# Optimization experiments

Measured on AMD Instinct MI355X. Metric: run time of the kernel, lower is better.

The kernel has to match this reference:

```python
import jax, jax.numpy as jnp
import numpy as np

B, T, NCH, DFF = 64, 480, 32, 32   # batch, seq_len+pred_len, d_model, d_ff
LAYERS = 3                          # conv_layers
NFFT, WIN, HOP = 64, 64, 4
FRAMES = T // HOP + 1               # 121 == (seq_len+pred_len+hop)/hop


def _stft(x):
    # x: [B, N, T] real -> (re, im) each [B, N, NFFT, FRAMES]
    # torch.stft(center=True, pad_mode='reflect', normalized=True, onesided=False)
    pad = NFFT // 2
    xp = jnp.pad(x, ((0, 0), (0, 0), (pad, pad)), mode='reflect')
    idx = jnp.arange(FRAMES)[:, None] * HOP + jnp.arange(NFFT)[None, :]
    win = 0.5 * (1.0 - jnp.cos(2.0 * jnp.pi * jnp.arange(WIN, dtype=jnp.float32) / WIN))  # periodic hann
    frames = xp[:, :, idx] * win                      # [B, N, FRAMES, NFFT]
    spec = jnp.fft.fft(frames, axis=-1) / jnp.sqrt(jnp.float32(NFFT))
    spec = jnp.swapaxes(spec, -1, -2)                 # [B, N, NFFT, FRAMES]
    return spec.real.astype(x.dtype), spec.imag.astype(x.dtype)


def _conv2d(x, w, b, dil, pad):
    y = jax.lax.conv_general_dilated(
        x, w, window_strides=(1, 1), padding=[(pad, pad), (pad, pad)],
        rhs_dilation=(dil, dil), dimension_numbers=('NCHW', 'OIHW', 'NCHW'))
    return y + b[None, :, None, None]


def _cconv(xr, xi, wr, wi, br, bi, dil, pad):
    # apply_complexConv2D: fr(re) - fi(im) + 1j*(fr(im) + fi(re)), biases included in each apply
    rr = _conv2d(xr, wr, br, dil, pad)
    ri = _conv2d(xi, wr, br, dil, pad)
    ir = _conv2d(xr, wi, bi, dil, pad)
    ii = _conv2d(xi, wi, bi, dil, pad)
    return rr - ii, ri + ir


def _cmul(order, ar, ai, br, bi):
    return (jnp.einsum(order, ar, br) - jnp.einsum(order, ai, bi),
            jnp.einsum(order, ar, bi) + jnp.einsum(order, ai, br))


def reference(x, w0r, w0i, b0r, b0i, W1r, W1i, B1r, B1i, W2r, W2i, B2r, B2i, w_l0, b_l0, w_l2, b_l2):
    xt = jnp.swapaxes(x, 1, 2)                         # [B, N, T]
    sr, si = _stft(xt)                                 # [B, N, F, K]
    qkr, qki = _cmul('bnfk,bngk->bnfg', sr, si, sr, si)
    qkr, qki = jax.nn.sigmoid(qkr), jax.nn.sigmoid(qki)
    ar, ai = _cmul('bnfg,bngk->bnfk', qkr, qki, sr, si)

    outs_r, outs_i = [], []
    r0, i0 = _cconv(ar, ai, w0r, w0i, b0r, b0i, 1, 0)  # 1x1 complex conv
    outs_r.append(jax.nn.relu(r0)); outs_i.append(jax.nn.relu(i0))
    for k in range(1, LAYERS):                          # dilated 3x3 complex conv pairs
        j = k - 1
        hr, hi = _cconv(ar, ai, W1r[j], W1i[j], B1r[j], B1i[j], k, k)
        hr, hi = _cconv(hr, hi, W2r[j], W2i[j], B2r[j], B2i[j], k, k)
        outs_r.append(jax.nn.relu(hr)); outs_i.append(jax.nn.relu(hi))
    mr = sum(outs_r) / LAYERS
    mi = sum(outs_i) / LAYERS

    # l0: Linear(2 -> 1) over stacked [real, imag]
    cr = mr * w_l0[0, 0] + mi * w_l0[0, 1] + b_l0[0]    # [B, N, F, K]
    h = cr.mean(axis=2)                                 # [B, N, K]
    y = jnp.einsum('bnk,tk->bnt', h, w_l2) + b_l2       # l2: Linear(FRAMES -> T)
    return jnp.transpose(y, (0, 2, 1))                  # [B, T, N]


def setup_inputs() -> dict:
    key = jax.random.key(0)
    ks = jax.random.split(key, 18)
    s1 = 1.0 / np.sqrt(NCH)          # 1x1 conv fan-in
    s3 = 1.0 / np.sqrt(NCH * 9)      # 3x3 conv fan-in
    return {
        'x':   jax.random.normal(ks[0], (B, T, NCH), jnp.float32),
        'w0r': jax.random.normal(ks[1], (NCH, NCH, 1, 1), jnp.float32) * s1,
        'w0i': jax.random.normal(ks[2], (NCH, NCH, 1, 1), jnp.float32) * s1,
        'b0r': jax.random.normal(ks[3], (NCH,), jnp.float32) * 0.01,
        'b0i': jax.random.normal(ks[4], (NCH,), jnp.float32) * 0.01,
        'W1r': jax.random.normal(ks[5], (LAYERS - 1, DFF, NCH, 3, 3), jnp.float32) * s3,
        'W1i': jax.random.normal(ks[6], (LAYERS - 1, DFF, NCH, 3, 3), jnp.float32) * s3,
        'B1r': jax.random.normal(ks[7], (LAYERS - 1, DFF), jnp.float32) * 0.01,
        'B1i': jax.random.normal(ks[8], (LAYERS - 1, DFF), jnp.float32) * 0.01,
        'W2r': jax.random.normal(ks[9], (LAYERS - 1, NCH, DFF, 3, 3), jnp.float32) * s3,
        'W2i': jax.random.normal(ks[10], (LAYERS - 1, NCH, DFF, 3, 3), jnp.float32) * s3,
        'B2r': jax.random.normal(ks[11], (LAYERS - 1, NCH), jnp.float32) * 0.01,
        'B2i': jax.random.normal(ks[12], (LAYERS - 1, NCH), jnp.float32) * 0.01,
        'w_l0': jax.random.normal(ks[13], (1, 2), jnp.float32) * 0.5,
        'b_l0': jax.random.normal(ks[14], (1,), jnp.float32) * 0.01,
        'w_l2': jax.random.normal(ks[15], (T, FRAMES), jnp.float32) * (1.0 / np.sqrt(FRAMES)),
        'b_l2': jax.random.normal(ks[16], (T,), jnp.float32) * 0.01,
    }
```

## Files before the change

kernel.cpp:

```cpp
#include <hip/hip_runtime.h>
#include <hip/hip_bf16.h>


typedef __attribute__((ext_vector_type(8))) short bf16x8;
typedef __attribute__((ext_vector_type(4))) short bf16x4;
typedef __attribute__((ext_vector_type(4))) float f32x4;

__device__ __forceinline__ ushort f2bf(float v) {
  __hip_bfloat16 h = __float2bfloat16(v);
  return *reinterpret_cast<ushort*>(&h);
}
__device__ __forceinline__ float bf2f_raw(ushort u) {
  union { uint i; float f; } c; c.i = ((uint)u) << 16; return c.f;
}
__device__ __forceinline__ void split_bf(float v, ushort& h, ushort& l) {
  h = f2bf(v); l = f2bf(v - bf2f_raw(h));
}
__device__ __forceinline__ bf16x8 mk8(bf16x4 a, bf16x4 b) {
  bf16x8 r;
  r[0]=a[0]; r[1]=a[1]; r[2]=a[2]; r[3]=a[3];
  r[4]=b[0]; r[5]=b[1]; r[6]=b[2]; r[7]=b[3];
  return r;
}
__device__ __forceinline__ void gld16(const ushort* g, char* lds) {
  __builtin_amdgcn_global_load_lds(
      (const __attribute__((address_space(1))) void*)g,
      (__attribute__((address_space(3))) void*)lds, 16, 0, 0);
}

#define MFMA16(A,B,C) __builtin_amdgcn_mfma_f32_16x16x32_bf16(A, B, C, 0, 0, 0)
#define SPMACC(acc, Ah, Al, Bh, Bl)      \
  acc = MFMA16(Ah, Bh, acc);             \
  acc = MFMA16(Al, Bh, acc);             \
  acc = MFMA16(Ah, Bl, acc);

__global__ __launch_bounds__(512) void stft_mfma_k(const float* __restrict__ x,
                                                   const ushort* __restrict__ WF,
                                                   ushort* __restrict__ ap) {
  __shared__ __align__(16) char smem[133376];
  const int bid = blockIdx.x;
  const int b = bid >> 5, n = bid & 31;
  const int tid = threadIdx.x;
  ushort* xph = reinterpret_cast<ushort*>(smem + 131072);
  ushort* xpl = xph + 576;

  for (int i = tid; i < 576; i += 512) {
    float v = 0.f;
    if (i < 544) {
      int p = i - 32;
      if (p < 0) p = -p;
      if (p >= 480) p = 958 - p;
      v = x[(b * 480 + p) * 32 + n];
    }
    ushort h, l; split_bf(v, h, l);
    xph[i] = h; xpl[i] = l;
  }
  __syncthreads();

  const int wv = tid >> 6, lane = tid & 63;
  const int mt = wv >> 1, nth = wv & 1;
  const int l15 = lane & 15, l4 = lane >> 4;

  bf16x8 WA[2][2][2];
#pragma unroll
  for (int cs = 0; cs < 2; ++cs)
#pragma unroll
    for (int part = 0; part < 2; ++part)
#pragma unroll
      for (int ks = 0; ks < 2; ++ks)
        WA[cs][part][ks] = *reinterpret_cast<const bf16x8*>(
            WF + (((cs * 2 + part) * 2 + ks) * 4 + mt) * 512 + lane * 8);

  f32x4 acc1[2][4];
#pragma unroll
  for (int cs = 0; cs < 2; ++cs)
#pragma unroll
    for (int nt = 0; nt < 4; ++nt) acc1[cs][nt] = (f32x4){0.f, 0.f, 0.f, 0.f};

#pragma unroll
  for (int ks = 0; ks < 2; ++ks) {
    bf16x8 bh[4], bl[4];
#pragma unroll
    for (int nt = 0; nt < 4; ++nt) {
      int n_ = ((nth * 4 + nt) * 16) + l15;
      int e = n_ * 4 + ks * 32 + l4 * 8;
      bf16x4 h0 = *reinterpret_cast<const bf16x4*>(xph + e);
      bf16x4 h1 = *reinterpret_cast<const bf16x4*>(xph + e + 4);
      bf16x4 l0 = *reinterpret_cast<const bf16x4*>(xpl + e);
      bf16x4 l1 = *reinterpret_cast<const bf16x4*>(xpl + e + 4);
      bh[nt] = mk8(h0, h1); bl[nt] = mk8(l0, l1);
    }
#pragma unroll
    for (int cs = 0; cs < 2; ++cs)
#pragma unroll
      for (int nt = 0; nt < 4; ++nt) {
        SPMACC(acc1[cs][nt], WA[cs][0][ks], WA[cs][1][ks], bh[nt], bl[nt]);
      }
  }

#pragma unroll
  for (int cs = 0; cs < 2; ++cs)
#pragma unroll
    for (int nt = 0; nt < 4; ++nt) {
      int k = (nth * 4 + nt) * 16 + l15;
      bool kv = (k < 121);
#pragma unroll
      for (int r = 0; r < 4; ++r) {
        int f = mt * 16 + l4 * 4 + r;
        float v = kv ? acc1[cs][nt][r] : 0.f;
        ushort h, l; split_bf(v, h, l);
        int ba = (f << 8) + (k << 1); ba ^= (f & 7) << 4;
        *reinterpret_cast<ushort*>(smem + cs * 32768 + ba) = h;
        *reinterpret_cast<ushort*>(smem + cs * 32768 + 16384 + ba) = l;
        int bt = (k << 7) + (f << 1); bt ^= (k & 7) << 4;
        *reinterpret_cast<ushort*>(smem + 65536 + cs * 32768 + bt) = h;
        *reinterpret_cast<ushort*>(smem + 65536 + cs * 32768 + 16384 + bt) = l;
      }
    }
  __syncthreads();

  f32x4 acc2[2][4];
#pragma unroll
  for (int nt = 0; nt < 2; ++nt)
#pragma unroll
    for (int c = 0; c < 4; ++c) acc2[nt][c] = (f32x4){0.f, 0.f, 0.f, 0.f};

#pragma unroll
  for (int ks = 0; ks < 4; ++ks) {
    bf16x8 A_[2][2];
#pragma unroll
    for (int comp = 0; comp < 2; ++comp)
#pragma unroll
      for (int part = 0; part < 2; ++part) {
        int f = mt * 16 + l15;
        int ba = (f << 8) + ((ks * 32 + l4 * 8) << 1); ba ^= (f & 7) << 4;
        A_[comp][part] = *reinterpret_cast<const bf16x8*>(smem + comp * 32768 + part * 16384 + ba);
      }
    bf16x8 B_[2][2][2];
#pragma unroll
    for (int comp = 0; comp < 2; ++comp)
#pragma unroll
      for (int part = 0; part < 2; ++part)
#pragma unroll
        for (int nt = 0; nt < 2; ++nt) {
          int g = (nth * 2 + nt) * 16 + l15;
          int ba = (g << 8) + ((ks * 32 + l4 * 8) << 1); ba ^= (g & 7) << 4;
          B_[comp][part][nt] = *reinterpret_cast<const bf16x8*>(smem + comp * 32768 + part * 16384 + ba);
        }
#pragma unroll
    for (int nt = 0; nt < 2; ++nt) {
      SPMACC(acc2[nt][0], A_[0][0], A_[0][1], B_[0][0][nt], B_[0][1][nt]);
      SPMACC(acc2[nt][1], A_[1][0], A_[1][1], B_[1][0][nt], B_[1][1][nt]);
      SPMACC(acc2[nt][2], A_[0][0], A_[0][1], B_[1][0][nt], B_[1][1][nt]);
      SPMACC(acc2[nt][3], A_[1][0], A_[1][1], B_[0][0][nt], B_[0][1][nt]);
    }
  }
  __syncthreads();

#pragma unroll
  for (int nt = 0; nt < 2; ++nt) {
    int g = (nth * 2 + nt) * 16 + l15;
#pragma unroll
    for (int r = 0; r < 4; ++r) {
      int f = mt * 16 + l4 * 4 + r;
      float qr = acc2[nt][0][r] - acc2[nt][1][r];
      float qi = acc2[nt][2][r] + acc2[nt][3][r];
      float vr = 1.f / (1.f + __expf(-qr));
      float vi = 1.f / (1.f + __expf(-qi));
      int ba = (f << 7) + (g << 1); ba ^= (f & 7) << 4;
      ushort h, l;
      split_bf(vr, h, l);
      *reinterpret_cast<ushort*>(smem + ba) = h;
      *reinterpret_cast<ushort*>(smem + 8192 + ba) = l;
      split_bf(vi, h, l);
      *reinterpret_cast<ushort*>(smem + 16384 + ba) = h;
      *reinterpret_cast<ushort*>(smem + 24576 + ba) = l;
    }
  }
  __syncthreads();

  f32x4 acc3[4][3];
#pragma unroll
  for (int nt = 0; nt < 4; ++nt)
#pragma unroll
    for (int c = 0; c < 3; ++c) acc3[nt][c] = (f32x4){0.f, 0.f, 0.f, 0.f};

#pragma unroll
  for (int ks = 0; ks < 2; ++ks) {
    bf16x8 QA[2][2];
#pragma unroll
    for (int comp = 0; comp < 2; ++comp)
#pragma unroll
      for (int part = 0; part < 2; ++part) {
        int f = mt * 16 + l15;
        int ba = (f << 7) + ((ks * 32 + l4 * 8) << 1); ba ^= (f & 7) << 4;
        QA[comp][part] = *reinterpret_cast<const bf16x8*>(smem + comp * 16384 + part * 8192 + ba);
      }
#pragma unroll
    for (int nt = 0; nt < 4; ++nt) {
      int k = (nth * 4 + nt) * 16 + l15;
      int bq = (k << 7) + ((ks * 32 + l4 * 8) << 1); bq ^= (k & 7) << 4;
      bf16x8 Srh = *reinterpret_cast<const bf16x8*>(smem + 65536 + bq);
      bf16x8 Srl = *reinterpret_cast<const bf16x8*>(smem + 81920 + bq);
      bf16x8 Sih = *reinterpret_cast<const bf16x8*>(smem + 98304 + bq);
      bf16x8 Sil = *reinterpret_cast<const bf16x8*>(smem + 114688 + bq);
      SPMACC(acc3[nt][0], QA[0][0], QA[0][1], Srh, Srl);
      SPMACC(acc3[nt][1], QA[1][0], QA[1][1], Sih, Sil);
      SPMACC(acc3[nt][2], QA[0][0], QA[0][1], Sih, Sil);
      SPMACC(acc3[nt][2], QA[1][0], QA[1][1], Srh, Srl);
    }
  }
  __syncthreads();

#pragma unroll
  for (int nt = 0; nt < 4; ++nt) {
    int k = (nth * 4 + nt) * 16 + l15;
#pragma unroll
    for (int r = 0; r < 4; ++r) {
      int f = mt * 16 + l4 * 4 + r;
      float ar = acc3[nt][0][r] - acc3[nt][1][r];
      float ai = acc3[nt][2][r];
      int ba = (f << 8) + (k << 1); ba ^= (f & 7) << 4;
      *reinterpret_cast<ushort*>(smem + ba) = f2bf(ar);
      *reinterpret_cast<ushort*>(smem + 16384 + ba) = f2bf(ai);
    }
  }
  __syncthreads();

  uint4* dst = reinterpret_cast<uint4*>(ap);
  for (int i = tid; i < 2048; i += 512) {
    int comp = i >> 10, rem = i & 1023;
    int f = rem >> 4, q = rem & 15;
    uint4 v = *reinterpret_cast<const uint4*>(
        smem + comp * 16384 + (f << 8) + ((q ^ (f & 7)) << 4));
    dst[((size_t)(b * 64 + n + 32 * comp) * 64) * 16 + rem] = v;
  }
}

__global__ __launch_bounds__(256) void transpose_k(const ushort* __restrict__ ap,
    ushort* __restrict__ an, const ushort* __restrict__ AF,
    const float* __restrict__ BB, const float* __restrict__ wl0,
    float* __restrict__ csumA) {
  __shared__ __align__(16) ushort T[64 * 128];
  const int b = blockIdx.x >> 6, h = blockIdx.x & 63;
  const int tid = threadIdx.x;
#pragma unroll
  for (int it = 0; it < 4; ++it) {
    int i = it * 256 + tid;
    int cc = i >> 4, q = i & 15;
    const uint4* src = reinterpret_cast<const uint4*>(ap) +
                       ((size_t)((b * 64 + cc) * 64 + h) * 16 + q);
    *reinterpret_cast<uint4*>(&T[cc * 128 + q * 8]) = *src;
  }
  __syncthreads();
  const int p = tid >> 1, cc0 = (tid & 1) * 32;
  uint ou[16];
#pragma unroll
  for (int it = 0; it < 16; ++it) {
    uint lo = T[(cc0 + 2 * it) * 128 + p];
    uint hi = T[(cc0 + 2 * it + 1) * 128 + p];
    ou[it] = lo | (hi << 16);
  }
  uint4* dst = reinterpret_cast<uint4*>(an + ((size_t)((b * 64 + h) * 128 + p) * 64 + cc0));
#pragma unroll
  for (int r = 0; r < 4; ++r) dst[r] = make_uint4(ou[4*r], ou[4*r+1], ou[4*r+2], ou[4*r+3]);
  __syncthreads();

  char* S = reinterpret_cast<char*>(T);
#pragma unroll
  for (int it = 0; it < 16; ++it) {
    int byt = p * 128 + (cc0 + 2 * it) * 2;
    byt ^= (p & 7) << 4;
    *reinterpret_cast<uint*>(S + byt) = ou[it];
  }
  __syncthreads();

  const int wave = tid >> 6, lane = tid & 63;
  const int mtb = wave & 1, ntb = (wave >> 1) * 4;
  const int l15 = lane & 15, l4 = lane >> 4;
  const ushort* Ab = AF + lane * 8;
  bf16x8 AH[2][2], AL[2][2];
#pragma unroll
  for (int ks = 0; ks < 2; ++ks)
#pragma unroll
    for (int mi = 0; mi < 2; ++mi) {
      AH[ks][mi] = *reinterpret_cast<const bf16x8*>(Ab + ks * 2048 + (mtb + 2 * mi) * 512);
      AL[ks][mi] = *reinterpret_cast<const bf16x8*>(Ab + 4096 + ks * 2048 + (mtb + 2 * mi) * 512);
    }
  f32x4 acc[2][4];
#pragma unroll
  for (int mi = 0; mi < 2; ++mi)
#pragma unroll
    for (int nt = 0; nt < 4; ++nt) acc[mi][nt] = (f32x4){0.f, 0.f, 0.f, 0.f};
#pragma unroll
  for (int ks = 0; ks < 2; ++ks) {
    bf16x8 bv[4];
#pragma unroll
    for (int nt = 0; nt < 4; ++nt) {
      int w = (ntb + nt) * 16 + l15;
      int byt = w * 128 + ks * 64 + l4 * 16;
      byt ^= (w & 7) << 4;
      bv[nt] = *reinterpret_cast<const bf16x8*>(S + byt);
    }
#pragma unroll
    for (int nt = 0; nt < 4; ++nt) {
      acc[0][nt] = MFMA16(AH[ks][0], bv[nt], acc[0][nt]);
      acc[1][nt] = MFMA16(AH[ks][1], bv[nt], acc[1][nt]);
    }
#pragma unroll
    for (int nt = 0; nt < 4; ++nt) {
      acc[0][nt] = MFMA16(AL[ks][0], bv[nt], acc[0][nt]);
      acc[1][nt] = MFMA16(AL[ks][1], bv[nt], acc[1][nt]);
    }
  }
  const float w00 = wl0[0], w01 = wl0[1];
#pragma unroll
  for (int nt = 0; nt < 4; ++nt) {
    int gw = (ntb + nt) * 16 + l15;
    if (gw < 121) {
#pragma unroll
      for (int r = 0; r < 4; ++r) {
        int n = mtb * 16 + l4 * 4 + r;
        float rr = acc[0][nt][r] + BB[n];
        float im = acc[1][nt][r] + BB[n + 32];
        csumA[((size_t)(b * 32 + n) * 64 + h) * 121 + gw] =
            (fmaxf(rr, 0.f) * w00 + fmaxf(im, 0.f) * w01) * (1.f / 3.f);
      }
    }
  }
}

__global__ __launch_bounds__(256) void prep_k(
    const float* __restrict__ w0r, const float* __restrict__ w0i,
    const float* __restrict__ b0r, const float* __restrict__ b0i,
    const float* __restrict__ W1r, const float* __restrict__ W1i,
    const float* __restrict__ B1r, const float* __restrict__ B1i,
    const float* __restrict__ W2r, const float* __restrict__ W2i,
    const float* __restrict__ B2r, const float* __restrict__ B2i,
    const float* __restrict__ wl2,
    ushort* __restrict__ AF, ushort* __restrict__ WF, float* __restrict__ BB,
    float* __restrict__ wl2T, float* __restrict__ zpg) {
  const int blk = blockIdx.x, tid = threadIdx.x;
  const float PI32 = 0.0981747704246810387f;

  if (blk == 38) {
    for (int i = tid; i < 121 * 480; i += 256) {
      int k = i / 480, t = i - k * 480;
      wl2T[i] = wl2[t * 121 + k];
    }
    if (tid < 16) zpg[tid] = 0.f;
    return;
  }
  if (blk == 37) {
    for (int i = tid; i < 16384; i += 256) {
      int j = i & 7, ln = (i >> 3) & 63, mt = (i >> 9) & 3, ks = (i >> 11) & 1;
      int part = (i >> 12) & 1, cs = (i >> 13) & 1;
      int f = mt * 16 + (ln & 15);
      int t = ks * 32 + (ln >> 4) * 8 + j;
      float win = 0.5f * (1.0f - __cosf(PI32 * (float)t));
      int m = (f * t) & 63;
      float sv, cv;
      __sincosf(PI32 * (float)m, &sv, &cv);
      float val = (cs == 0) ? (win * cv * 0.125f) : (-win * sv * 0.125f);
      ushort h = f2bf(val);
      WF[i] = part ? f2bf(val - bf2f_raw(h)) : h;
    }
    return;
  }

  int conv, tap, TT;
  const float *Wr, *Wi;
  if (blk == 0) { conv = 0; tap = 0; TT = 1; Wr = w0r; Wi = w0i; }
  else {
    int q = blk - 1; conv = 1 + q / 9; tap = q - (q / 9) * 9; TT = 9;
    if (conv == 1)      { Wr = W1r;        Wi = W1i; }
    else if (conv == 2) { Wr = W2r;        Wi = W2i; }
    else if (conv == 3) { Wr = W1r + 9216; Wi = W1i + 9216; }
    else                { Wr = W2r + 9216; Wi = W2i + 9216; }
  }
  ushort thi[16], tlo[16];
#pragma unroll
  for (int jj = 0; jj < 16; ++jj) {
    int e = tid * 16 + jj;
    int j = e & 7, lane_e = (e >> 3) & 63, mt = (e >> 9) & 3, ks = (e >> 11) & 1;
    int o  = mt * 16 + (lane_e & 15);
    int cc = ks * 32 + 8 * (lane_e >> 4) + j;
    int ci = cc & 31, ch = cc >> 5, on = o & 31, oh = o >> 5;
    float wr = Wr[(on * 32 + ci) * TT + tap];
    float wi = Wi[(on * 32 + ci) * TT + tap];
    float v = (oh == 0) ? (ch == 0 ? wr : -wi) : (ch == 0 ? wi : wr);
    ushort h = f2bf(v);
    thi[jj] = h;
    tlo[jj] = f2bf(v - bf2f_raw(h));
  }
  ushort* base = AF + conv * 73728 + tap * 8192 + tid * 16;
  uint4* dh = reinterpret_cast<uint4*>(base);
  uint4* dl = reinterpret_cast<uint4*>(base + 4096);
  dh[0] = *reinterpret_cast<uint4*>(&thi[0]);
  dh[1] = *reinterpret_cast<uint4*>(&thi[8]);
  dl[0] = *reinterpret_cast<uint4*>(&tlo[0]);
  dl[1] = *reinterpret_cast<uint4*>(&tlo[8]);

  if (blk == 0) {
    for (int i = tid; i < 320; i += 256) {
      int c = i >> 6, o = i & 63;
      const float *br, *bi;
      if (c == 0)      { br = b0r;      bi = b0i; }
      else if (c == 1) { br = B1r;      bi = B1i; }
      else if (c == 2) { br = B2r;      bi = B2i; }
      else if (c == 3) { br = B1r + 32; bi = B1i + 32; }
      else             { br = B2r + 32; bi = B2i + 32; }
      BB[c * 64 + o] = (o < 32) ? (br[o] - bi[o]) : (br[o - 32] + bi[o - 32]);
    }
  }
}

#define RWB 8704

__device__ __forceinline__ void run_taps9(const char* __restrict__ smem,
    const ushort* __restrict__ afrag, int d,
    int ng, int mtb, int l15, int l4, int lane, f32x4 acc[2][8]) {
  const ushort* Ab = afrag + lane * 8;
#pragma unroll
  for (int t = 0; t < 9; ++t) {
    const int dy = t / 3;
    const int dxo = ((t - dy * 3) - 1) * d;
    const int bufb = (dy - 1) * d + 2 + ng * 2;
    const ushort* At = Ab + t * 8192;
    bf16x8 AH[2][2], AL[2][2];
#pragma unroll
    for (int ks = 0; ks < 2; ++ks)
#pragma unroll
      for (int mi = 0; mi < 2; ++mi) {
        AH[ks][mi] = *reinterpret_cast<const bf16x8*>(At + ks * 2048 + (mtb + 2 * mi) * 512);
        AL[ks][mi] = *reinterpret_cast<const bf16x8*>(At + 4096 + ks * 2048 + (mtb + 2 * mi) * 512);
      }
#pragma unroll
    for (int ks = 0; ks < 2; ++ks) {
      bf16x8 bv[8];
#pragma unroll
      for (int nt = 0; nt < 8; ++nt) {
        int bw = (nt & 3) * 16 + l15 + dxo + 2;
        int byt = (bufb + (nt >> 2)) * RWB + bw * 128 + ks * 64 + l4 * 16;
        byt ^= (bw & 7) << 4;
        bv[nt] = *reinterpret_cast<const bf16x8*>(smem + byt);
      }
      __builtin_amdgcn_s_setprio(1);
#pragma unroll
      for (int nt = 0; nt < 8; ++nt) {
        acc[0][nt] = MFMA16(AH[ks][0], bv[nt], acc[0][nt]);
        acc[1][nt] = MFMA16(AH[ks][1], bv[nt], acc[1][nt]);
      }
#pragma unroll
      for (int nt = 0; nt < 8; ++nt) {
        acc[0][nt] = MFMA16(AL[ks][0], bv[nt], acc[0][nt]);
        acc[1][nt] = MFMA16(AL[ks][1], bv[nt], acc[1][nt]);
      }
      __builtin_amdgcn_s_setprio(0);
    }
  }
}

__device__ __forceinline__ void conv_body3(char* smem,
    const ushort* __restrict__ xin, ushort* __restrict__ tout,
    const ushort* __restrict__ afrag, const float* __restrict__ bb,
    const float* __restrict__ wl0, float* __restrict__ csum,
    const ushort* __restrict__ zp,
    int d, int b, int h0, int side, int mode, int tid) {
  const int wave = tid >> 6, lane = tid & 63;
  const int mtb = wave & 1;
  const int ng = wave >> 1;
  const int l15 = lane & 15, l4 = lane >> 4;
  const int wbase = side * 64;

#pragma unroll
  for (int r = 0; r < 8; ++r) {
    const int hh = h0 + r - 2;
    const bool hv = ((unsigned)hh < 64u);
    const ushort* rowp = xin + ((size_t)(b * 64 + hh) << 13);
#pragma unroll
    for (int c = 0; c < 3; ++c) {
      int i = c * 256 + tid;
      if (i < 544) {
        int bw = i >> 3, q = i & 7;
        int gw = wbase + bw - 2;
        int qs = q ^ (bw & 7);
        const ushort* src = (hv && (unsigned)gw < 128u)
                                ? (rowp + (size_t)gw * 64 + qs * 8)
                                : zp;
        char* ldsb = smem + r * RWB + ((i & ~63) << 4);
        gld16(src, ldsb);
      }
    }
  }
  __syncthreads();

  f32x4 acc[2][8];
#pragma unroll
  for (int mi = 0; mi < 2; ++mi)
#pragma unroll
    for (int nt = 0; nt < 8; ++nt) acc[mi][nt] = (f32x4){0.f, 0.f, 0.f, 0.f};

  run_taps9(smem, afrag, d, ng, mtb, l15, l4, lane, acc);

  if (mode == 2) {
    __syncthreads();
    uint* Lb = reinterpret_cast<uint*>(smem);
#pragma unroll
    for (int mi = 0; mi < 2; ++mi) {
#pragma unroll
      for (int rp = 0; rp < 2; ++rp) {
        int o = (mtb + 2 * mi) * 16 + l4 * 4 + rp * 2;
        float b0 = bb[o], b1 = bb[o + 1];
#pragma unroll
        for (int nt = 0; nt < 8; ++nt) {
          int jrow = ng * 2 + (nt >> 2);
          int wl = (nt & 3) * 16 + l15;
          uint pk = (uint)f2bf(acc[mi][nt][rp * 2] + b0) |
                    ((uint)f2bf(acc[mi][nt][rp * 2 + 1] + b1) << 16);
          Lb[(jrow * 32 + (o >> 1)) * 66 + wl] = pk;
        }
      }
    }
    __syncthreads();
#pragma unroll
    for (int c = 0; c < 8; ++c) {
      int i = c * 256 + tid;
      int jrow = i >> 9, rem = i & 511;
      int wl = rem >> 3, q = rem & 7;
      int gw = wbase + wl;
      int hh = h0 + jrow;
      bool val = (gw < 121);
      uint4 v;
      v.x = val ? Lb[(jrow * 32 + q * 4 + 0) * 66 + wl] : 0u;
      v.y = val ? Lb[(jrow * 32 + q * 4 + 1) * 66 + wl] : 0u;
      v.z = val ? Lb[(jrow * 32 + q * 4 + 2) * 66 + wl] : 0u;
      v.w = val ? Lb[(jrow * 32 + q * 4 + 3) * 66 + wl] : 0u;
      *reinterpret_cast<uint4*>(
          tout + (((size_t)(b * 64 + hh) * 128 + gw) * 64 + q * 8)) = v;
    }
  } else {
    const float w00 = wl0[0], w01 = wl0[1];
#pragma unroll
    for (int nt = 0; nt < 8; ++nt) {
      int gw = wbase + (nt & 3) * 16 + l15;
      int hh = h0 + ng * 2 + (nt >> 2);
      if (gw < 121) {
#pragma unroll
        for (int r = 0; r < 4; ++r) {
          int n = mtb * 16 + l4 * 4 + r;
          float rr = acc[0][nt][r] + bb[n];
          float im = acc[1][nt][r] + bb[n + 32];
          float v = (fmaxf(rr, 0.f) * w00 + fmaxf(im, 0.f) * w01) * (1.f / 3.f);
          float* p = csum + ((size_t)(b * 32 + n) * 64 + hh) * 121 + gw;
          if (mode == 1) v += *p;
          *p = v;
        }
      }
    }
  }
}

__global__ __launch_bounds__(256, 2) void convD1_k(
    const ushort* __restrict__ an, ushort* __restrict__ t1, ushort* __restrict__ t2,
    const ushort* __restrict__ AF, const float* __restrict__ BB,
    const float* __restrict__ wl0, const ushort* __restrict__ zp) {
  __shared__ __align__(16) char smem[8 * RWB];
  const int x = blockIdx.x & 7, j = blockIdx.x >> 3;
  const int role = j & 1, sub = j >> 1;
  const int wg = (x << 8) | sub;
  const int b = wg >> 5, rem = wg & 31;
  const int h0 = ((rem >> 1) & 15) * 4, side = rem & 1;
  const int tid = threadIdx.x;
  if (role == 0)
    conv_body3(smem, an, t1, AF + 1 * 73728, BB + 64, wl0, nullptr, zp, 1, b, h0, side, 2, tid);
  else
    conv_body3(smem, an, t2, AF + 3 * 73728, BB + 192, wl0, nullptr, zp, 2, b, h0, side, 2, tid);
}

__global__ __launch_bounds__(256, 2) void convD2_k(
    const ushort* __restrict__ t1, const ushort* __restrict__ t2,
    const ushort* __restrict__ AF, const float* __restrict__ BB,
    const float* __restrict__ wl0, float* __restrict__ csumA,
    float* __restrict__ csumB, const ushort* __restrict__ zp) {
  __shared__ __align__(16) char smem[8 * RWB];
  const int x = blockIdx.x & 7, j = blockIdx.x >> 3;
  const int role = j & 1, sub = j >> 1;
  const int wg = (x << 8) | sub;
  const int b = wg >> 5, rem = wg & 31;
  const int h0 = ((rem >> 1) & 15) * 4, side = rem & 1;
  const int tid = threadIdx.x;
  if (role == 0)
    conv_body3(smem, t1, nullptr, AF + 2 * 73728, BB + 128, wl0, csumA, zp, 1, b, h0, side, 1, tid);
  else
    conv_body3(smem, t2, nullptr, AF + 4 * 73728, BB + 256, wl0, csumB, zp, 2, b, h0, side, 0, tid);
}

__global__ __launch_bounds__(256) void epi_k(const float* __restrict__ csumA,
    const float* __restrict__ csumB,
    const float* __restrict__ bl0, const float* __restrict__ wl2T,
    const float* __restrict__ bl2, float* __restrict__ out) {
  const int b = blockIdx.x >> 5, n = blockIdx.x & 31;
  __shared__ float sh[121];
  const int tid = threadIdx.x;
  const float* baseA = csumA + (size_t)(b * 32 + n) * 64 * 121;
  const float* baseB = csumB + (size_t)(b * 32 + n) * 64 * 121;
  for (int k = tid; k < 121; k += 256) {
    float s = 0.f;
#pragma unroll 8
    for (int f = 0; f < 64; ++f) s += baseA[f * 121 + k] + baseB[f * 121 + k];
    sh[k] = s * (1.f / 64.f) + bl0[0];
  }
  __syncthreads();
  for (int t = tid; t < 480; t += 256) {
    float acc = bl2[t];
#pragma unroll 8
    for (int k = 0; k < 121; ++k) acc = fmaf(sh[k], wl2T[k * 480 + t], acc);
    out[(b * 480 + t) * 32 + n] = acc;
  }
}

extern "C" void kernel_launch(void* const* d_in, const int* in_sizes, int n_in,
                              void* d_out, int out_size, void* d_ws, size_t ws_size,
                              hipStream_t stream) {
  const float* x   = (const float*)d_in[0];
  const float* w0r = (const float*)d_in[1];
  const float* w0i = (const float*)d_in[2];
  const float* b0r = (const float*)d_in[3];
  const float* b0i = (const float*)d_in[4];
  const float* W1r = (const float*)d_in[5];
  const float* W1i = (const float*)d_in[6];
  const float* B1r = (const float*)d_in[7];
  const float* B1i = (const float*)d_in[8];
  const float* W2r = (const float*)d_in[9];
  const float* W2i = (const float*)d_in[10];
  const float* B2r = (const float*)d_in[11];
  const float* B2i = (const float*)d_in[12];
  const float* wl0 = (const float*)d_in[13];
  const float* bl0 = (const float*)d_in[14];
  const float* wl2 = (const float*)d_in[15];
  const float* bl2 = (const float*)d_in[16];

  char* ws = (char*)d_ws;
  const size_t MB64 = (size_t)64 << 20;
  ushort* ap    = (ushort*)ws;
  ushort* t2    = (ushort*)ws;
  ushort* an    = (ushort*)(ws + MB64);
  float*  csumB = (float*)(ws + MB64);
  ushort* t1    = (ushort*)(ws + 2 * MB64);
  float*  csumA = (float*)(ws + 3 * MB64);
  const size_t CSZ = (size_t)64 * 32 * 64 * 121 * 4;
  ushort* AF   = (ushort*)(ws + 3 * MB64 + CSZ);
  ushort* WFp  = AF + 5 * 73728;
  float*  BB   = (float*)(WFp + 16384);
  float*  wl2T = BB + 320;
  float*  zpg  = wl2T + 58080;
  float*  out  = (float*)d_out;

  hipLaunchKernelGGL(prep_k, dim3(39), dim3(256), 0, stream,
                     w0r, w0i, b0r, b0i, W1r, W1i, B1r, B1i, W2r, W2i, B2r, B2i,
                     wl2, AF, WFp, BB, wl2T, zpg);
  hipLaunchKernelGGL(stft_mfma_k, dim3(2048), dim3(512), 0, stream, x, WFp, ap);
  hipLaunchKernelGGL(transpose_k, dim3(4096), dim3(256), 0, stream,
                     ap, an, AF, BB, wl0, csumA);
  hipLaunchKernelGGL(convD1_k, dim3(4096), dim3(256), 0, stream,
                     an, t1, t2, AF, BB, wl0, (const ushort*)zpg);
  hipLaunchKernelGGL(convD2_k, dim3(4096), dim3(256), 0, stream,
                     t1, t2, AF, BB, wl0, csumA, csumB, (const ushort*)zpg);
  hipLaunchKernelGGL(epi_k, dim3(2048), dim3(256), 0, stream,
                     csumA, csumB, bl0, wl2T, bl2, out);
}
```

Baseline: 501.1 us.

## Share staged input tile across both dilated convs in convD1 and store directly

convD1 now stages each input tile into LDS once and runs both the dilation-1 and dilation-2 convolutions on it inside one block. This halves the grid and removes the duplicate global loads of the shared input. The LDS-transpose epilogue is replaced by direct 8-byte packed bf16 stores from registers to t1/t2, which drops two barriers and the LDS round trip but gives less coalesced global writes. Each block now does twice the MFMA work, so there are fewer blocks available to hide latency.

```diff
diff --git a/kernel.cpp b/kernel.cpp
--- a/kernel.cpp
+++ b/kernel.cpp
@@ -417,62 +417,9 @@
 
 #define RWB 8704
 
-__device__ __forceinline__ void run_taps9(const char* __restrict__ smem,
-    const ushort* __restrict__ afrag, int d,
-    int ng, int mtb, int l15, int l4, int lane, f32x4 acc[2][8]) {
-  const ushort* Ab = afrag + lane * 8;
-#pragma unroll
-  for (int t = 0; t < 9; ++t) {
-    const int dy = t / 3;
-    const int dxo = ((t - dy * 3) - 1) * d;
-    const int bufb = (dy - 1) * d + 2 + ng * 2;
-    const ushort* At = Ab + t * 8192;
-    bf16x8 AH[2][2], AL[2][2];
-#pragma unroll
-    for (int ks = 0; ks < 2; ++ks)
-#pragma unroll
-      for (int mi = 0; mi < 2; ++mi) {
-        AH[ks][mi] = *reinterpret_cast<const bf16x8*>(At + ks * 2048 + (mtb + 2 * mi) * 512);
-        AL[ks][mi] = *reinterpret_cast<const bf16x8*>(At + 4096 + ks * 2048 + (mtb + 2 * mi) * 512);
-      }
-#pragma unroll
-    for (int ks = 0; ks < 2; ++ks) {
-      bf16x8 bv[8];
-#pragma unroll
-      for (int nt = 0; nt < 8; ++nt) {
-        int bw = (nt & 3) * 16 + l15 + dxo + 2;
-        int byt = (bufb + (nt >> 2)) * RWB + bw * 128 + ks * 64 + l4 * 16;
-        byt ^= (bw & 7) << 4;
-        bv[nt] = *reinterpret_cast<const bf16x8*>(smem + byt);
-      }
-      __builtin_amdgcn_s_setprio(1);
-#pragma unroll
-      for (int nt = 0; nt < 8; ++nt) {
-        acc[0][nt] = MFMA16(AH[ks][0], bv[nt], acc[0][nt]);
-        acc[1][nt] = MFMA16(AH[ks][1], bv[nt], acc[1][nt]);
-      }
-#pragma unroll
-      for (int nt = 0; nt < 8; ++nt) {
-        acc[0][nt] = MFMA16(AL[ks][0], bv[nt], acc[0][nt]);
-        acc[1][nt] = MFMA16(AL[ks][1], bv[nt], acc[1][nt]);
-      }
-      __builtin_amdgcn_s_setprio(0);
-    }
-  }
-}
-
-__device__ __forceinline__ void conv_body3(char* smem,
-    const ushort* __restrict__ xin, ushort* __restrict__ tout,
-    const ushort* __restrict__ afrag, const float* __restrict__ bb,
-    const float* __restrict__ wl0, float* __restrict__ csum,
-    const ushort* __restrict__ zp,
-    int d, int b, int h0, int side, int mode, int tid) {
-  const int wave = tid >> 6, lane = tid & 63;
-  const int mtb = wave & 1;
-  const int ng = wave >> 1;
-  const int l15 = lane & 15, l4 = lane >> 4;
-  const int wbase = side * 64;
-
+__device__ __forceinline__ void stage8(char* smem,
+    const ushort* __restrict__ xin, const ushort* __restrict__ zp,
+    int b, int h0, int wbase, int tid) {
 #pragma unroll
   for (int r = 0; r < 8; ++r) {
     const int hh = h0 + r - 2;
@@ -493,70 +440,48 @@
       }
     }
   }
-  __syncthreads();
-
-  f32x4 acc[2][8];
-#pragma unroll
-  for (int mi = 0; mi < 2; ++mi)
-#pragma unroll
-    for (int nt = 0; nt < 8; ++nt) acc[mi][nt] = (f32x4){0.f, 0.f, 0.f, 0.f};
-
-  run_taps9(smem, afrag, d, ng, mtb, l15, l4, lane, acc);
-
-  if (mode == 2) {
-    __syncthreads();
-    uint* Lb = reinterpret_cast<uint*>(smem);
-#pragma unroll
-    for (int mi = 0; mi < 2; ++mi) {
-#pragma unroll
-      for (int rp = 0; rp < 2; ++rp) {
-        int o = (mtb + 2 * mi) * 16 + l4 * 4 + rp * 2;
-        float b0 = bb[o], b1 = bb[o + 1];
-#pragma unroll
-        for (int nt = 0; nt < 8; ++nt) {
-          int jrow = ng * 2 + (nt >> 2);
-          int wl = (nt & 3) * 16 + l15;
-          uint pk = (uint)f2bf(acc[mi][nt][rp * 2] + b0) |
-                    ((uint)f2bf(acc[mi][nt][rp * 2 + 1] + b1) << 16);
-          Lb[(jrow * 32 + (o >> 1)) * 66 + wl] = pk;
-        }
-      }
-    }
-    __syncthreads();
-#pragma unroll
-    for (int c = 0; c < 8; ++c) {
-      int i = c * 256 + tid;
-      int jrow = i >> 9, rem = i & 511;
-      int wl = rem >> 3, q = rem & 7;
-      int gw = wbase + wl;
-      int hh = h0 + jrow;
-      bool val = (gw < 121);
-      uint4 v;
-      v.x = val ? Lb[(jrow * 32 + q * 4 + 0) * 66 + wl] : 0u;
-      v.y = val ? Lb[(jrow * 32 + q * 4 + 1) * 66 + wl] : 0u;
-      v.z = val ? Lb[(jrow * 32 + q * 4 + 2) * 66 + wl] : 0u;
-      v.w = val ? Lb[(jrow * 32 + q * 4 + 3) * 66 + wl] : 0u;
-      *reinterpret_cast<uint4*>(
-          tout + (((size_t)(b * 64 + hh) * 128 + gw) * 64 + q * 8)) = v;
-    }
-  } else {
-    const float w00 = wl0[0], w01 = wl0[1];
-#pragma unroll
-    for (int nt = 0; nt < 8; ++nt) {
-      int gw = wbase + (nt & 3) * 16 + l15;
-      int hh = h0 + ng * 2 + (nt >> 2);
-      if (gw < 121) {
-#pragma unroll
-        for (int r = 0; r < 4; ++r) {
-          int n = mtb * 16 + l4 * 4 + r;
-          float rr = acc[0][nt][r] + bb[n];
-          float im = acc[1][nt][r] + bb[n + 32];
-          float v = (fmaxf(rr, 0.f) * w00 + fmaxf(im, 0.f) * w01) * (1.f / 3.f);
-          float* p = csum + ((size_t)(b * 32 + n) * 64 + hh) * 121 + gw;
-          if (mode == 1) v += *p;
-          *p = v;
-        }
-      }
+}
+
+__device__ __forceinline__ void run_taps9(const char* __restrict__ smem,
+    const ushort* __restrict__ afrag, int d,
+    int ng, int mtb, int l15, int l4, int lane, f32x4 acc[2][8]) {
+  const ushort* Ab = afrag + lane * 8;
+#pragma unroll
+  for (int t = 0; t < 9; ++t) {
+    const int dy = t / 3;
+    const int dxo = ((t - dy * 3) - 1) * d;
+    const int bufb = (dy - 1) * d + 2 + ng * 2;
+    const ushort* At = Ab + t * 8192;
+    bf16x8 AH[2][2], AL[2][2];
+#pragma unroll
+    for (int ks = 0; ks < 2; ++ks)
+#pragma unroll
+      for (int mi = 0; mi < 2; ++mi) {
+        AH[ks][mi] = *reinterpret_cast<const bf16x8*>(At + ks * 2048 + (mtb + 2 * mi) * 512);
+        AL[ks][mi] = *reinterpret_cast<const bf16x8*>(At + 4096 + ks * 2048 + (mtb + 2 * mi) * 512);
+      }
+#pragma unroll
+    for (int ks = 0; ks < 2; ++ks) {
+      bf16x8 bv[8];
+#pragma unroll
+      for (int nt = 0; nt < 8; ++nt) {
+        int bw = (nt & 3) * 16 + l15 + dxo + 2;
+        int byt = (bufb + (nt >> 2)) * RWB + bw * 128 + ks * 64 + l4 * 16;
+        byt ^= (bw & 7) << 4;
+        bv[nt] = *reinterpret_cast<const bf16x8*>(smem + byt);
+      }
+      __builtin_amdgcn_s_setprio(1);
+#pragma unroll
+      for (int nt = 0; nt < 8; ++nt) {
+        acc[0][nt] = MFMA16(AH[ks][0], bv[nt], acc[0][nt]);
+        acc[1][nt] = MFMA16(AH[ks][1], bv[nt], acc[1][nt]);
+      }
+#pragma unroll
+      for (int nt = 0; nt < 8; ++nt) {
+        acc[0][nt] = MFMA16(AL[ks][0], bv[nt], acc[0][nt]);
+        acc[1][nt] = MFMA16(AL[ks][1], bv[nt], acc[1][nt]);
+      }
+      __builtin_amdgcn_s_setprio(0);
     }
   }
 }
@@ -564,18 +489,97 @@
 __global__ __launch_bounds__(256, 2) void convD1_k(
     const ushort* __restrict__ an, ushort* __restrict__ t1, ushort* __restrict__ t2,
     const ushort* __restrict__ AF, const float* __restrict__ BB,
-    const float* __restrict__ wl0, const ushort* __restrict__ zp) {
+    const ushort* __restrict__ zp) {
   __shared__ __align__(16) char smem[8 * RWB];
   const int x = blockIdx.x & 7, j = blockIdx.x >> 3;
-  const int role = j & 1, sub = j >> 1;
-  const int wg = (x << 8) | sub;
+  const int wg = (x << 8) | j;
   const int b = wg >> 5, rem = wg & 31;
   const int h0 = ((rem >> 1) & 15) * 4, side = rem & 1;
   const int tid = threadIdx.x;
-  if (role == 0)
-    conv_body3(smem, an, t1, AF + 1 * 73728, BB + 64, wl0, nullptr, zp, 1, b, h0, side, 2, tid);
-  else
-    conv_body3(smem, an, t2, AF + 3 * 73728, BB + 192, wl0, nullptr, zp, 2, b, h0, side, 2, tid);
+  const int wave = tid >> 6, lane = tid & 63;
+  const int mtb = wave & 1, ng = wave >> 1;
+  const int l15 = lane & 15, l4 = lane >> 4;
+  const int wbase = side * 64;
+
+  stage8(smem, an, zp, b, h0, wbase, tid);
+  __syncthreads();
+
+#pragma unroll
+  for (int role = 0; role < 2; ++role) {
+    const int d = role + 1;
+    const ushort* afrag = AF + (role == 0 ? 1 : 3) * 73728;
+    const float* bb = BB + (role == 0 ? 64 : 192);
+    ushort* tout = (role == 0) ? t1 : t2;
+
+    f32x4 acc[2][8];
+#pragma unroll
+    for (int mi = 0; mi < 2; ++mi)
+#pragma unroll
+      for (int nt = 0; nt < 8; ++nt) acc[mi][nt] = (f32x4){0.f, 0.f, 0.f, 0.f};
+
+    run_taps9(smem, afrag, d, ng, mtb, l15, l4, lane, acc);
+
+#pragma unroll
+    for (int mi = 0; mi < 2; ++mi) {
+      const int o0 = (mtb + 2 * mi) * 16 + l4 * 4;
+      const float b0 = bb[o0], b1 = bb[o0 + 1], b2 = bb[o0 + 2], b3 = bb[o0 + 3];
+#pragma unroll
+      for (int nt = 0; nt < 8; ++nt) {
+        const int w = wbase + (nt & 3) * 16 + l15;
+        const int hh = h0 + ng * 2 + (nt >> 2);
+        uint2 pk = make_uint2(0u, 0u);
+        if (w < 121) {
+          pk.x = (uint)f2bf(acc[mi][nt][0] + b0) |
+                 ((uint)f2bf(acc[mi][nt][1] + b1) << 16);
+          pk.y = (uint)f2bf(acc[mi][nt][2] + b2) |
+                 ((uint)f2bf(acc[mi][nt][3] + b3) << 16);
+        }
+        *reinterpret_cast<uint2*>(
+            tout + (((size_t)(b * 64 + hh) * 128 + w) * 64 + o0)) = pk;
+      }
+    }
+  }
+}
+
+__device__ __forceinline__ void conv_csum(char* smem,
+    const ushort* __restrict__ xin, const ushort* __restrict__ afrag,
+    const float* __restrict__ bb, const float* __restrict__ wl0,
+    float* __restrict__ csum, const ushort* __restrict__ zp,
+    int d, int b, int h0, int side, int mode, int tid) {
+  const int wave = tid >> 6, lane = tid & 63;
+  const int mtb = wave & 1, ng = wave >> 1;
+  const int l15 = lane & 15, l4 = lane >> 4;
+  const int wbase = side * 64;
+
+  stage8(smem, xin, zp, b, h0, wbase, tid);
+  __syncthreads();
+
+  f32x4 acc[2][8];
+#pragma unroll
+  for (int mi = 0; mi < 2; ++mi)
+#pragma unroll
+    for (int nt = 0; nt < 8; ++nt) acc[mi][nt] = (f32x4){0.f, 0.f, 0.f, 0.f};
+
+  run_taps9(smem, afrag, d, ng, mtb, l15, l4, lane, acc);
+
+  const float w00 = wl0[0], w01 = wl0[1];
+#pragma unroll
+  for (int nt = 0; nt < 8; ++nt) {
+    int gw = wbase + (nt & 3) * 16 + l15;
+    int hh = h0 + ng * 2 + (nt >> 2);
+    if (gw < 121) {
+#pragma unroll
+      for (int r = 0; r < 4; ++r) {
+        int n = mtb * 16 + l4 * 4 + r;
+        float rr = acc[0][nt][r] + bb[n];
+        float im = acc[1][nt][r] + bb[n + 32];
+        float v = (fmaxf(rr, 0.f) * w00 + fmaxf(im, 0.f) * w01) * (1.f / 3.f);
+        float* p = csum + ((size_t)(b * 32 + n) * 64 + hh) * 121 + gw;
+        if (mode == 1) v += *p;
+        *p = v;
+      }
+    }
+  }
 }
 
 __global__ __launch_bounds__(256, 2) void convD2_k(
@@ -591,9 +595,9 @@
   const int h0 = ((rem >> 1) & 15) * 4, side = rem & 1;
   const int tid = threadIdx.x;
   if (role == 0)
-    conv_body3(smem, t1, nullptr, AF + 2 * 73728, BB + 128, wl0, csumA, zp, 1, b, h0, side, 1, tid);
+    conv_csum(smem, t1, AF + 2 * 73728, BB + 128, wl0, csumA, zp, 1, b, h0, side, 1, tid);
   else
-    conv_body3(smem, t2, nullptr, AF + 4 * 73728, BB + 256, wl0, csumB, zp, 2, b, h0, side, 0, tid);
+    conv_csum(smem, t2, AF + 4 * 73728, BB + 256, wl0, csumB, zp, 2, b, h0, side, 0, tid);
 }
 
 __global__ __launch_bounds__(256) void epi_k(const float* __restrict__ csumA,
@@ -663,8 +667,8 @@
   hipLaunchKernelGGL(stft_mfma_k, dim3(2048), dim3(512), 0, stream, x, WFp, ap);
   hipLaunchKernelGGL(transpose_k, dim3(4096), dim3(256), 0, stream,
                      ap, an, AF, BB, wl0, csumA);
-  hipLaunchKernelGGL(convD1_k, dim3(4096), dim3(256), 0, stream,
-                     an, t1, t2, AF, BB, wl0, (const ushort*)zpg);
+  hipLaunchKernelGGL(convD1_k, dim3(2048), dim3(256), 0, stream,
+                     an, t1, t2, AF, BB, (const ushort*)zpg);
   hipLaunchKernelGGL(convD2_k, dim3(4096), dim3(256), 0, stream,
                      t1, t2, AF, BB, wl0, csumA, csumB, (const ushort*)zpg);
   hipLaunchKernelGGL(epi_k, dim3(2048), dim3(256), 0, stream,
```

New measurement: 520.1 us. 1.04x slower.
